# Performance work log

Hardware: AMD Instinct MI355X
Metric: run time of the kernel (lower is better)

## Reference

```python
import jax, jax.numpy as jnp
import numpy as np

B, DIM, H, W = 8, 128, 192, 192
HEADS = 4
WS = 8        # window size
SHIFT = 4     # shift size
N = WS * WS   # tokens per window
HD = DIM // HEADS
NW = (H // WS) * (W // WS)


def _relative_position_index(ws):
    coords = np.stack(np.meshgrid(np.arange(ws), np.arange(ws), indexing='ij'))  # (2,ws,ws)
    cf = coords.reshape(2, -1)                                                   # (2,N)
    rel = cf[:, :, None] - cf[:, None, :]                                        # (2,N,N)
    rel = rel.transpose(1, 2, 0).astype(np.int64)                                # (N,N,2)
    rel[:, :, 0] += ws - 1
    rel[:, :, 1] += ws - 1
    rel[:, :, 0] *= 2 * ws - 1
    return rel.sum(-1)  # (N,N)


def _window_partition_np(x, ws):
    b, h, w, c = x.shape
    x = x.reshape(b, h // ws, ws, w // ws, ws, c)
    return x.transpose(0, 1, 3, 2, 4, 5).reshape(-1, ws, ws, c)


def _shift_mask(h, w, ws, shift):
    img_mask = np.zeros((1, h, w, 1), dtype=np.float32)
    slices = (slice(0, -ws), slice(-ws, -shift), slice(-shift, None))
    cnt = 0
    for hs in slices:
        for wsl in slices:
            img_mask[:, hs, wsl, :] = cnt
            cnt += 1
    mw = _window_partition_np(img_mask, ws).reshape(-1, ws * ws)  # (nW, N)
    attn_mask = mw[:, None, :] - mw[:, :, None]                    # (nW, N, N)
    return np.where(attn_mask != 0, -100.0, 0.0).astype(np.float32)


_RPI = jnp.asarray(_relative_position_index(WS))   # (N,N) int
_MASK = jnp.asarray(_shift_mask(H, W, WS, SHIFT))  # (nW,N,N)


def setup_inputs() -> dict:
    key = jax.random.key(0)
    k0, k1, k2, k3 = jax.random.split(key, 4)
    return {
        'x': jax.random.normal(k0, (B, DIM, H, W), jnp.float32),
        'qkv_w': jax.random.normal(k1, (3 * DIM, DIM), jnp.float32) * 0.02,
        'qkv_b': jnp.zeros((3 * DIM,), jnp.float32),
        'proj_w': jax.random.normal(k2, (DIM, DIM), jnp.float32) * 0.02,
        'proj_b': jnp.zeros((DIM,), jnp.float32),
        'rpb_table': jax.random.normal(k3, ((2 * WS - 1) ** 2, HEADS), jnp.float32) * 0.02,
    }


def reference(x, qkv_w, qkv_b, proj_w, proj_b, rpb_table):
    scale = HD ** -0.5
    # (B,C,H,W) -> (B,H,W,C)
    xs = jnp.transpose(x, (0, 2, 3, 1))
    # cyclic shift
    xs = jnp.roll(xs, shift=(-SHIFT, -SHIFT), axis=(1, 2))
    # window partition -> (B*nW, N, C)
    win = xs.reshape(B, H // WS, WS, W // WS, WS, DIM)
    win = jnp.transpose(win, (0, 1, 3, 2, 4, 5)).reshape(B * NW, N, DIM)
    # qkv projection
    qkv = win @ qkv_w.T + qkv_b                                   # (B_,N,3C)
    qkv = qkv.reshape(B * NW, N, 3, HEADS, HD)
    qkv = jnp.transpose(qkv, (2, 0, 3, 1, 4))                     # (3,B_,h,N,d)
    q, k, v = qkv[0], qkv[1], qkv[2]
    attn = jnp.einsum('bhnd,bhmd->bhnm', q * scale, k)            # (B_,h,N,N)
    # relative position bias
    bias = rpb_table[_RPI.reshape(-1)].reshape(N, N, HEADS)
    bias = jnp.transpose(bias, (2, 0, 1))                         # (h,N,N)
    attn = attn + bias[None]
    # shift mask per window
    attn = attn.reshape(B, NW, HEADS, N, N) + _MASK[None, :, None]
    attn = jax.nn.softmax(attn.reshape(B * NW, HEADS, N, N), axis=-1)
    out = jnp.einsum('bhnm,bhmd->bhnd', attn, v)                  # (B_,h,N,d)
    out = jnp.transpose(out, (0, 2, 1, 3)).reshape(B * NW, N, DIM)
    out = out @ proj_w.T + proj_b
    # window reverse -> (B,H,W,C)
    out = out.reshape(B, H // WS, W // WS, WS, WS, DIM)
    out = jnp.transpose(out, (0, 1, 3, 2, 4, 5)).reshape(B, H, W, DIM)
    # reverse cyclic shift
    out = jnp.roll(out, shift=(SHIFT, SHIFT), axis=(1, 2))
    return jnp.transpose(out, (0, 3, 1, 2))  # (B,C,H,W)
```

## Files before the change

kernel.cpp:

```cpp
#include <hip/hip_runtime.h>

#define HIMG 192
#define HWSZ (192*192)
#define NWX  24

typedef __bf16 bf16;
typedef __bf16 bf16x4 __attribute__((ext_vector_type(4)));
typedef __bf16 bf16x8 __attribute__((ext_vector_type(8)));
typedef float  f32x4  __attribute__((ext_vector_type(4)));

#define MFMA(a,b,c) __builtin_amdgcn_mfma_f32_16x16x32_bf16((a),(b),(c),0,0,0)
#define SW(r) (((((r)&7) ^ ((((r)>>3)&1)<<2))) << 4)

static __device__ __forceinline__ bf16x8 ldg8(const float* p) {
    const float4 u = ((const float4*)p)[0];
    const float4 v = ((const float4*)p)[1];
    bf16x8 r;
    r[0]=(bf16)u.x; r[1]=(bf16)u.y; r[2]=(bf16)u.z; r[3]=(bf16)u.w;
    r[4]=(bf16)v.x; r[5]=(bf16)v.y; r[6]=(bf16)v.z; r[7]=(bf16)v.w;
    return r;
}
template<int WSB>
static __device__ __forceinline__ bf16x8 ldw(const float* wf, const bf16* wh, int off) {
    if (WSB) return *(const bf16x8*)(wh + off);
    return ldg8(wf + off);
}
static __device__ __forceinline__ bf16x4 pk4b(f32x4 v, float4 b) {
    bf16x4 r; r[0]=(bf16)(v[0]+b.x); r[1]=(bf16)(v[1]+b.y);
    r[2]=(bf16)(v[2]+b.z); r[3]=(bf16)(v[3]+b.w); return r;
}
static __device__ __forceinline__ bf16x4 pk4bs(f32x4 v, float4 b, float s) {
    bf16x4 r; r[0]=(bf16)((v[0]+b.x)*s); r[1]=(bf16)((v[1]+b.y)*s);
    r[2]=(bf16)((v[2]+b.z)*s); r[3]=(bf16)((v[3]+b.w)*s); return r;
}
static __device__ __forceinline__ bf16x4 pk4c(f32x4 v, float b) {
    bf16x4 r; r[0]=(bf16)(v[0]+b); r[1]=(bf16)(v[1]+b);
    r[2]=(bf16)(v[2]+b); r[3]=(bf16)(v[3]+b); return r;
}
static __device__ __forceinline__ bf16x4 pk4s(f32x4 v, float s) {
    bf16x4 r; r[0]=(bf16)(v[0]*s); r[1]=(bf16)(v[1]*s);
    r[2]=(bf16)(v[2]*s); r[3]=(bf16)(v[3]*s); return r;
}
static __device__ __forceinline__ bf16x4 pk4(f32x4 v) {
    bf16x4 r; r[0]=(bf16)v[0]; r[1]=(bf16)v[1]; r[2]=(bf16)v[2]; r[3]=(bf16)v[3]; return r;
}
static __device__ __forceinline__ bf16x8 cat8(bf16x4 a, bf16x4 b) {
    bf16x8 r; r[0]=a[0]; r[1]=a[1]; r[2]=a[2]; r[3]=a[3];
    r[4]=b[0]; r[5]=b[1]; r[6]=b[2]; r[7]=b[3]; return r;
}

__global__ __launch_bounds__(256) void setup_ws(const float* __restrict__ rpb,
                                                const float* __restrict__ qkv_w,
                                                const float* __restrict__ proj_w,
                                                float* __restrict__ wbias,
                                                bf16* __restrict__ hqkv,
                                                bf16* __restrict__ hproj,
                                                float* __restrict__ wbf,
                                                bf16* __restrict__ hqkvf,
                                                bf16* __restrict__ hprojf) {
    const int e = blockIdx.x * 256 + threadIdx.x;
    if (e < 16384) {
        const int h = e >> 12, i = (e >> 6) & 63, j = e & 63;
        const int dy = (i >> 3) - (j >> 3) + 7;
        const int dx = (i & 7)  - (j & 7)  + 7;
        wbias[e] = rpb[(dy * 15 + dx) * 4 + h];
    } else if (e < 65536) {
        const int i = e - 16384;
        hqkv[i] = (bf16)qkv_w[i];
    } else if (e < 81920) {
        const int i = e - 65536;
        hproj[i] = (bf16)proj_w[i];
    } else if (e < 98304) {
        const int t = e - 81920;
        const int r = t & 3, lane = (t >> 2) & 63;
        const int m = (t >> 8) & 3, n = (t >> 10) & 3, h = t >> 12;
        const int lo = lane & 15, hi = lane >> 4;
        const int i_ = n*16 + lo;
        const int j_ = (m >> 1)*32 + hi*8 + (m & 1)*4 + r;
        const int dy = (i_ >> 3) - (j_ >> 3) + 7;
        const int dx = (i_ & 7)  - (j_ & 7)  + 7;
        wbf[t] = rpb[(dy * 15 + dx) * 4 + h];
    } else if (e < 147456) {
        const int t = e - 98304;
        const int el = t & 7, lane = (t >> 3) & 63;
        const int a = (t >> 9) & 1, kb = (t >> 10) & 3;
        const int h = (t >> 12) & 3, ph = t >> 14;
        const int lo = lane & 15, hi = lane >> 4;
        const int prow = ((lo >> 2) << 3) + (lo & 3);
        const int row = (ph == 2) ? (256 + h*32 + a*16 + lo)
                                  : (ph*128 + h*32 + prow + a*4);
        const int col = kb*32 + hi*8 + el;
        hqkvf[t] = (bf16)qkv_w[row*128 + col];
    } else {
        const int t = e - 147456;
        const int el = t & 7, lane = (t >> 3) & 63;
        const int tA = (t >> 9) & 3, kb = (t >> 11) & 3, oh = t >> 13;
        const int lo = lane & 15, hi = lane >> 4;
        const int row = oh*64 + tA*16 + lo;
        const int col = kb*32 + hi*8 + el;
        hprojf[t] = (bf16)proj_w[row*128 + col];
    }
}

__global__ __launch_bounds__(256, 3)
void qkv_attn(const float* __restrict__ x, const float* __restrict__ qkv_b,
              const bf16* __restrict__ hqkvf, const float* __restrict__ wbf,
              bf16* __restrict__ obuf)
{
    __shared__ char sX[16384];
    const int tid  = threadIdx.x;
    const int lane = tid & 63;
    const int h    = tid >> 6;
    const int lo   = lane & 15;
    const int hi   = lane >> 4;

    const int bid   = blockIdx.x;
    const int batch = bid & 7;
    const int wrem  = bid >> 3;
    const int wy    = wrem / NWX;
    const int wx    = wrem - wy * NWX;
    const long xbase = (long)batch * 128 * HWSZ;

    const f32x4 FZ = {0.f, 0.f, 0.f, 0.f};
    const float SCALE = 0.17677669529663687f;
    const int prow = ((lo >> 2) << 3) + (lo & 3);

    {
        int hh = wy*8 + (lane >> 3) + 4; if (hh >= HIMG) hh -= HIMG;
        int ww = wx*8 + (lane & 7)  + 4; if (ww >= HIMG) ww -= HIMG;
        const float* xp = x + xbase + hh * HIMG + ww;
        char* const wp = sX + lane * 256;
        const int swz = SW(lane);
        #pragma unroll
        for (int g = 0; g < 4; ++g) {
            const int c0 = h*32 + g*8;
            bf16x8 v;
            #pragma unroll
            for (int e = 0; e < 8; ++e) v[e] = (bf16)xp[(c0 + e) * HWSZ];
            *(bf16x8*)(wp + ((2*c0) ^ swz)) = v;
        }
    }
    __syncthreads();

    const bf16* const wQ = hqkvf + h * 4096;
    const bf16* const wK = hqkvf + 16384 + h * 4096;
    const bf16* const wV = hqkvf + 32768 + h * 4096;

    bf16x8 qf[4], kf[4], vf[2][2];

    {
        f32x4 acc[2][4];
        #pragma unroll
        for (int a = 0; a < 2; ++a)
            #pragma unroll
            for (int n = 0; n < 4; ++n) acc[a][n] = FZ;
        #pragma unroll
        for (int kb = 0; kb < 4; ++kb) {
            bf16x8 xf[4];
            #pragma unroll
            for (int n = 0; n < 4; ++n) {
                const int row = n*16 + lo;
                xf[n] = *(const bf16x8*)(sX + row*256 + ((kb*64 + hi*16) ^ SW(row)));
            }
            const bf16x8 w0 = *(const bf16x8*)(wQ + (kb*2    )*512 + lane*8);
            const bf16x8 w1 = *(const bf16x8*)(wQ + (kb*2 + 1)*512 + lane*8);
            #pragma unroll
            for (int n = 0; n < 4; ++n) {
                acc[0][n] = MFMA(w0, xf[n], acc[0][n]);
                acc[1][n] = MFMA(w1, xf[n], acc[1][n]);
            }
        }
        const float4 b0 = *(const float4*)(qkv_b + h*32 + hi*8);
        const float4 b1 = *(const float4*)(qkv_b + h*32 + hi*8 + 4);
        #pragma unroll
        for (int n = 0; n < 4; ++n)
            qf[n] = cat8(pk4bs(acc[0][n], b0, SCALE), pk4bs(acc[1][n], b1, SCALE));
    }

    {
        f32x4 ak[2][4], av[4][2];
        #pragma unroll
        for (int m = 0; m < 4; ++m) {
            ak[0][m] = FZ; ak[1][m] = FZ; av[m][0] = FZ; av[m][1] = FZ;
        }
        #pragma unroll
        for (int kb = 0; kb < 4; ++kb) {
            bf16x8 xf[4];
            #pragma unroll
            for (int m = 0; m < 4; ++m) {
                const int row = (m >> 1)*32 + (m & 1)*4 + prow;
                xf[m] = *(const bf16x8*)(sX + row*256 + ((kb*64 + hi*16) ^ SW(row)));
            }
            const bf16x8 wk0 = *(const bf16x8*)(wK + (kb*2    )*512 + lane*8);
            const bf16x8 wk1 = *(const bf16x8*)(wK + (kb*2 + 1)*512 + lane*8);
            const bf16x8 wv0 = *(const bf16x8*)(wV + (kb*2    )*512 + lane*8);
            const bf16x8 wv1 = *(const bf16x8*)(wV + (kb*2 + 1)*512 + lane*8);
            #pragma unroll
            for (int m = 0; m < 4; ++m) {
                ak[0][m] = MFMA(wk0, xf[m], ak[0][m]);
                ak[1][m] = MFMA(wk1, xf[m], ak[1][m]);
                av[m][0] = MFMA(xf[m], wv0, av[m][0]);
                av[m][1] = MFMA(xf[m], wv1, av[m][1]);
            }
        }
        const float4 b0 = *(const float4*)(qkv_b + 128 + h*32 + hi*8);
        const float4 b1 = *(const float4*)(qkv_b + 128 + h*32 + hi*8 + 4);
        #pragma unroll
        for (int m = 0; m < 4; ++m)
            kf[m] = cat8(pk4b(ak[0][m], b0), pk4b(ak[1][m], b1));
        const float bv0 = qkv_b[256 + h*32 + lo];
        const float bv1 = qkv_b[256 + h*32 + 16 + lo];
        #pragma unroll
        for (int kb = 0; kb < 2; ++kb) {
            vf[0][kb] = cat8(pk4c(av[kb*2][0], bv0), pk4c(av[kb*2 + 1][0], bv0));
            vf[1][kb] = cat8(pk4c(av[kb*2][1], bv1), pk4c(av[kb*2 + 1][1], bv1));
        }
    }

    const bool ey = (wy == 23), ex = (wx == 23);
    const bool edge = ey || ex;
    const float* const wbh = wbf + h * 4096;
    bf16x8 pf[2][4];
    float rinv[4];
    #pragma unroll
    for (int n = 0; n < 4; ++n) {
        const int i_ = n*16 + lo;
        const int yi = i_ >> 3, xi = i_ & 7;
        const int ri = (ey ? (yi < 4 ? 1 : 2) : 0) * 3 + (ex ? (xi < 4 ? 1 : 2) : 0);
        f32x4 sc[4];
        #pragma unroll
        for (int m = 0; m < 4; ++m) {
            f32x4 ci = *(const f32x4*)(wbh + (n*4 + m)*256 + lane*4);
            if (edge) {
                #pragma unroll
                for (int r = 0; r < 4; ++r) {
                    const int j_ = (m >> 1)*32 + hi*8 + (m & 1)*4 + r;
                    const int yj = j_ >> 3, xj = j_ & 7;
                    const int rj = (ey ? (yj < 4 ? 1 : 2) : 0) * 3 + (ex ? (xj < 4 ? 1 : 2) : 0);
                    ci[r] += (ri != rj) ? -100.0f : 0.0f;
                }
            }
            sc[m] = MFMA(kf[m], qf[n], ci);
        }
        float mx = -1e30f;
        #pragma unroll
        for (int m = 0; m < 4; ++m)
            #pragma unroll
            for (int r = 0; r < 4; ++r) mx = fmaxf(mx, sc[m][r]);
        mx = fmaxf(mx, __shfl_xor(mx, 16));
        mx = fmaxf(mx, __shfl_xor(mx, 32));
        float sum = 0.f;
        #pragma unroll
        for (int m = 0; m < 4; ++m)
            #pragma unroll
            for (int r = 0; r < 4; ++r) {
                const float p = __expf(sc[m][r] - mx);
                sc[m][r] = p; sum += p;
            }
        sum += __shfl_xor(sum, 16);
        sum += __shfl_xor(sum, 32);
        rinv[n] = 1.0f / sum;
        pf[0][n] = cat8(pk4(sc[0]), pk4(sc[1]));
        pf[1][n] = cat8(pk4(sc[2]), pk4(sc[3]));
    }

    f32x4 o0[2][4];
    #pragma unroll
    for (int o = 0; o < 2; ++o)
        #pragma unroll
        for (int n = 0; n < 4; ++n) o0[o][n] = FZ;
    #pragma unroll
    for (int kb = 0; kb < 2; ++kb)
        #pragma unroll
        for (int o = 0; o < 2; ++o)
            #pragma unroll
            for (int n = 0; n < 4; ++n)
                o0[o][n] = MFMA(vf[o][kb], pf[kb][n], o0[o][n]);

    bf16* const ob = obuf + (size_t)bid * 8192 + h * 2048;
    #pragma unroll
    for (int n = 0; n < 4; ++n)
        #pragma unroll
        for (int o = 0; o < 2; ++o)
            *(bf16x4*)(ob + (n*2 + o)*256 + lane*4) = pk4s(o0[o][n], rinv[n]);
}

__global__ __launch_bounds__(512, 3)
void proj_rows(const bf16* __restrict__ obuf, const bf16* __restrict__ hprojf,
               const float* __restrict__ proj_b, float* __restrict__ out)
{
    __shared__ char sR[49152];
    const int tid  = threadIdx.x;
    const int lane = tid & 63;
    const int wv   = tid >> 6;
    const int lo   = lane & 15;
    const int hi   = lane >> 4;

    const int bid   = blockIdx.x;
    const int batch = bid & 7;
    const int hh    = bid >> 3;
    int hr = hh + 188; if (hr >= 192) hr -= 192;
    const int wy = hr >> 3, iy = hr & 7;
    const int n_ = iy >> 1;

    #pragma unroll
    for (int k = 0; k < 6; ++k) {
        const int i  = tid + k*512;
        const int wr = i >> 4;
        const int cc = i & 15;
        const int wxx = wr >> 3, ix = wr & 7;
        const int win = (wy*NWX + wxx)*8 + batch;
        const int lo2 = (iy & 1)*8 + ix;
        const int hg = cc >> 2, oo = (cc >> 1) & 1, hp = cc & 1;
        const bf16* bp = obuf + (size_t)win*8192 + hg*2048 + (n_*2 + oo)*256;
        const bf16x4 p0 = *(const bf16x4*)(bp + ((hp*2    )*16 + lo2)*4);
        const bf16x4 p1 = *(const bf16x4*)(bp + ((hp*2 + 1)*16 + lo2)*4);
        int wo = wr + 4; if (wo >= 192) wo -= 192;
        *(bf16x8*)(sR + wo*256 + ((cc*16) ^ SW(wo))) = cat8(p0, p1);
    }
    __syncthreads();

    const int q  = wv >> 1;
    const int oh = wv & 1;
    const f32x4 FZ = {0.f, 0.f, 0.f, 0.f};
    f32x4 acc[4][3];
    #pragma unroll
    for (int tA = 0; tA < 4; ++tA)
        #pragma unroll
        for (int tN = 0; tN < 3; ++tN) acc[tA][tN] = FZ;

    #pragma unroll
    for (int kb = 0; kb < 4; ++kb) {
        bf16x8 of[3];
        #pragma unroll
        for (int tN = 0; tN < 3; ++tN) {
            const int tok = q*48 + tN*16 + lo;
            of[tN] = *(const bf16x8*)(sR + tok*256 + ((kb*64 + hi*16) ^ SW(tok)));
        }
        bf16x8 wf[4];
        #pragma unroll
        for (int tA = 0; tA < 4; ++tA)
            wf[tA] = *(const bf16x8*)(hprojf + (size_t)(((oh*4 + kb)*4 + tA)*64 + lane)*8);
        #pragma unroll
        for (int tA = 0; tA < 4; ++tA)
            #pragma unroll
            for (int tN = 0; tN < 3; ++tN)
                acc[tA][tN] = MFMA(of[tN], wf[tA], acc[tA][tN]);
    }

    #pragma unroll
    for (int tA = 0; tA < 4; ++tA) {
        const int oc = oh*64 + tA*16 + lo;
        const float pb = proj_b[oc];
        float* const orow = out + (size_t)(batch*128 + oc) * HWSZ + hh*192;
        #pragma unroll
        for (int tN = 0; tN < 3; ++tN) {
            const int tb = q*48 + tN*16 + hi*4;
            float4 v;
            v.x = acc[tA][tN][0] + pb;
            v.y = acc[tA][tN][1] + pb;
            v.z = acc[tA][tN][2] + pb;
            v.w = acc[tA][tN][3] + pb;
            *(float4*)(orow + tb) = v;
        }
    }
}

template<int WSB>
__global__ __launch_bounds__(64, 2)
void swin_fused(const float* __restrict__ x, const float* __restrict__ qkv_w,
                const float* __restrict__ qkv_b, const float* __restrict__ proj_w,
                const float* __restrict__ proj_b, const float* __restrict__ rpb,
                const float* __restrict__ wb, const bf16* __restrict__ hqkv,
                const bf16* __restrict__ hproj, float* __restrict__ out)
{
    __shared__ char sX[16384];

    const int lane = threadIdx.x & 63;
    const int lo   = lane & 15;
    const int hi   = lane >> 4;

    const int bid   = blockIdx.x;
    const int batch = bid & 7;
    const int wrem  = bid >> 3;
    const int wy    = wrem / NWX;
    const int wx    = wrem - wy * NWX;
    const long xbase = (long)batch * 128 * HWSZ;

    const f32x4 FZ = {0.f, 0.f, 0.f, 0.f};
    const float SCALE = 0.17677669529663687f;
    const int prow = ((lo >> 2) << 3) + (lo & 3);

    {
        int hh = wy*8 + (lane >> 3) + 4; if (hh >= HIMG) hh -= HIMG;
        int ww = wx*8 + (lane & 7)  + 4; if (ww >= HIMG) ww -= HIMG;
        const float* xp = x + xbase + hh * HIMG + ww;
        char* const wp = sX + lane * 256;
        const int swz = SW(lane);
        #pragma unroll
        for (int g = 0; g < 16; ++g) {
            bf16x8 v;
            #pragma unroll
            for (int e = 0; e < 8; ++e) v[e] = (bf16)xp[(g*8 + e) * HWSZ];
            *(bf16x8*)(wp + ((16*g) ^ swz)) = v;
        }
    }

    const bool ey = (wy == 23), ex = (wx == 23);
    const bool edge = ey || ex;

    bf16x4 ob[4][2][4];

    #pragma unroll
    for (int h = 0; h < 4; ++h) {
        bf16x8 qf[4], kf[4];
        {
            f32x4 acc[2][4];
            #pragma unroll
            for (int a = 0; a < 2; ++a)
                #pragma unroll
                for (int n = 0; n < 4; ++n) acc[a][n] = FZ;
            #pragma unroll
            for (int kb = 0; kb < 4; ++kb) {
                bf16x8 xf[4];
                #pragma unroll
                for (int n = 0; n < 4; ++n) {
                    const int row = n*16 + lo;
                    xf[n] = *(const bf16x8*)(sX + row*256 + ((kb*64 + hi*16) ^ SW(row)));
                }
                const int coff = kb*32 + hi*8;
                const bf16x8 w0 = ldw<WSB>(qkv_w, hqkv, (h*32 + prow    ) * 128 + coff);
                const bf16x8 w1 = ldw<WSB>(qkv_w, hqkv, (h*32 + prow + 4) * 128 + coff);
                #pragma unroll
                for (int n = 0; n < 4; ++n) {
                    acc[0][n] = MFMA(w0, xf[n], acc[0][n]);
                    acc[1][n] = MFMA(w1, xf[n], acc[1][n]);
                }
            }
            const float4 b0 = *(const float4*)(qkv_b + h*32 + hi*8);
            const float4 b1 = *(const float4*)(qkv_b + h*32 + hi*8 + 4);
            #pragma unroll
            for (int n = 0; n < 4; ++n)
                qf[n] = cat8(pk4bs(acc[0][n], b0, SCALE), pk4bs(acc[1][n], b1, SCALE));
        }
        {
            f32x4 ak[2][4];
            #pragma unroll
            for (int a = 0; a < 2; ++a)
                #pragma unroll
                for (int m = 0; m < 4; ++m) ak[a][m] = FZ;
            #pragma unroll
            for (int kb = 0; kb < 4; ++kb) {
                bf16x8 xf[4];
                #pragma unroll
                for (int m = 0; m < 4; ++m) {
                    const int row = (m >> 1)*32 + (m & 1)*4 + prow;
                    xf[m] = *(const bf16x8*)(sX + row*256 + ((kb*64 + hi*16) ^ SW(row)));
                }
                const int coff = kb*32 + hi*8;
                const bf16x8 w0 = ldw<WSB>(qkv_w, hqkv, (128 + h*32 + prow    ) * 128 + coff);
                const bf16x8 w1 = ldw<WSB>(qkv_w, hqkv, (128 + h*32 + prow + 4) * 128 + coff);
                #pragma unroll
                for (int m = 0; m < 4; ++m) {
                    ak[0][m] = MFMA(w0, xf[m], ak[0][m]);
                    ak[1][m] = MFMA(w1, xf[m], ak[1][m]);
                }
            }
            const float4 b0 = *(const float4*)(qkv_b + 128 + h*32 + hi*8);
            const float4 b1 = *(const float4*)(qkv_b + 128 + h*32 + hi*8 + 4);
            #pragma unroll
            for (int m = 0; m < 4; ++m)
                kf[m] = cat8(pk4b(ak[0][m], b0), pk4b(ak[1][m], b1));
        }

        f32x4 s2[4][4];
        const float* wbh = wb + h * 4096;
        #pragma unroll
        for (int n = 0; n < 4; ++n) {
            const int i_ = n*16 + lo;
            const int yi = i_ >> 3, xi = i_ & 7;
            const int ri = (ey ? (yi < 4 ? 1 : 2) : 0) * 3 + (ex ? (xi < 4 ? 1 : 2) : 0);
            #pragma unroll
            for (int m = 0; m < 4; ++m) {
                const int j0 = (m >> 1)*32 + hi*8 + (m & 1)*4;
                f32x4 ci;
                if (WSB) ci = *(const f32x4*)(wbh + i_*64 + j0);
                else {
                    #pragma unroll
                    for (int r = 0; r < 4; ++r) {
                        const int j_ = j0 + r;
                        ci[r] = rpb[((yi - (j_ >> 3) + 7) * 15 + (xi - (j_ & 7) + 7)) * 4 + h];
                    }
                }
                if (edge) {
                    #pragma unroll
                    for (int r = 0; r < 4; ++r) {
                        const int j_ = j0 + r;
                        const int yj = j_ >> 3, xj = j_ & 7;
                        const int rj = (ey ? (yj < 4 ? 1 : 2) : 0) * 3 + (ex ? (xj < 4 ? 1 : 2) : 0);
                        ci[r] += (ri != rj) ? -100.0f : 0.0f;
                    }
                }
                s2[m][n] = MFMA(kf[m], qf[n], ci);
            }
        }
        float rinv[4];
        #pragma unroll
        for (int n = 0; n < 4; ++n) {
            float mx = -1e30f;
            #pragma unroll
            for (int m = 0; m < 4; ++m)
                #pragma unroll
                for (int r = 0; r < 4; ++r) mx = fmaxf(mx, s2[m][n][r]);
            mx = fmaxf(mx, __shfl_xor(mx, 16));
            mx = fmaxf(mx, __shfl_xor(mx, 32));
            float sum = 0.f;
            #pragma unroll
            for (int m = 0; m < 4; ++m)
                #pragma unroll
                for (int r = 0; r < 4; ++r) {
                    const float p = __expf(s2[m][n][r] - mx);
                    s2[m][n][r] = p; sum += p;
                }
            sum += __shfl_xor(sum, 16);
            sum += __shfl_xor(sum, 32);
            rinv[n] = 1.0f / sum;
        }
        bf16x8 pf[2][4];
        #pragma unroll
        for (int kb = 0; kb < 2; ++kb)
            #pragma unroll
            for (int n = 0; n < 4; ++n)
                pf[kb][n] = cat8(pk4(s2[kb*2][n]), pk4(s2[kb*2 + 1][n]));

        bf16x8 vf[2][2];
        {
            f32x4 av[4][2];
            #pragma unroll
            for (int m = 0; m < 4; ++m) { av[m][0] = FZ; av[m][1] = FZ; }
            #pragma unroll
            for (int kb = 0; kb < 4; ++kb) {
                bf16x8 xv[4];
                #pragma unroll
                for (int m = 0; m < 4; ++m) {
                    const int row = (m >> 1)*32 + (m & 1)*4 + prow;
                    xv[m] = *(const bf16x8*)(sX + row*256 + ((kb*64 + hi*16) ^ SW(row)));
                }
                const int coff = kb*32 + hi*8;
                const bf16x8 w0 = ldw<WSB>(qkv_w, hqkv, (256 + h*32 + lo)      * 128 + coff);
                const bf16x8 w1 = ldw<WSB>(qkv_w, hqkv, (256 + h*32 + 16 + lo) * 128 + coff);
                #pragma unroll
                for (int m = 0; m < 4; ++m) {
                    av[m][0] = MFMA(xv[m], w0, av[m][0]);
                    av[m][1] = MFMA(xv[m], w1, av[m][1]);
                }
            }
            const float bv0 = qkv_b[256 + h*32 + lo];
            const float bv1 = qkv_b[256 + h*32 + 16 + lo];
            #pragma unroll
            for (int kb = 0; kb < 2; ++kb) {
                vf[0][kb] = cat8(pk4c(av[kb*2][0], bv0), pk4c(av[kb*2 + 1][0], bv0));
                vf[1][kb] = cat8(pk4c(av[kb*2][1], bv1), pk4c(av[kb*2 + 1][1], bv1));
            }
        }
        {
            f32x4 o0[2][4];
            #pragma unroll
            for (int o = 0; o < 2; ++o)
                #pragma unroll
                for (int n = 0; n < 4; ++n) o0[o][n] = FZ;
            #pragma unroll
            for (int kb = 0; kb < 2; ++kb)
                #pragma unroll
                for (int o = 0; o < 2; ++o)
                    #pragma unroll
                    for (int n = 0; n < 4; ++n)
                        o0[o][n] = MFMA(vf[o][kb], pf[kb][n], o0[o][n]);
            #pragma unroll
            for (int o = 0; o < 2; ++o)
                #pragma unroll
                for (int n = 0; n < 4; ++n)
                    ob[h][o][n] = pk4s(o0[o][n], rinv[n]);
        }
    }

    #pragma unroll
    for (int h = 0; h < 4; ++h)
        #pragma unroll
        for (int o = 0; o < 2; ++o) {
            const int cb = h*64 + o*32 + hi*8;
            #pragma unroll
            for (int n = 0; n < 4; ++n) {
                const int t = n*16 + lo;
                *(bf16x4*)(sX + t*256 + (cb ^ SW(t))) = ob[h][o][n];
            }
        }

    #pragma unroll
    for (int c4 = 0; c4 < 4; ++c4) {
        f32x4 pr[2][4];
        #pragma unroll
        for (int a = 0; a < 2; ++a)
            #pragma unroll
            for (int n = 0; n < 4; ++n) pr[a][n] = FZ;
        #pragma unroll
        for (int kb = 0; kb < 4; ++kb) {
            bf16x8 af[4];
            #pragma unroll
            for (int n = 0; n < 4; ++n) {
                const int row = n*16 + lo;
                af[n] = *(const bf16x8*)(sX + row*256 + ((kb*64 + hi*16) ^ SW(row)));
            }
            const int coff = kb*32 + hi*8;
            const bf16x8 w0 = ldw<WSB>(proj_w, hproj, (c4*32 + lo)      * 128 + coff);
            const bf16x8 w1 = ldw<WSB>(proj_w, hproj, (c4*32 + 16 + lo) * 128 + coff);
            #pragma unroll
            for (int n = 0; n < 4; ++n) {
                pr[0][n] = MFMA(w0, af[n], pr[0][n]);
                pr[1][n] = MFMA(w1, af[n], pr[1][n]);
            }
        }
        #pragma unroll
        for (int a = 0; a < 2; ++a) {
            const int ocb = c4*32 + a*16 + hi*4;
            const float4 pb = *(const float4*)(proj_b + ocb);
            #pragma unroll
            for (int n = 0; n < 4; ++n) {
                const int t = n*16 + lo;
                int hh = wy*8 + (t >> 3) + 4; if (hh >= HIMG) hh -= HIMG;
                int ww = wx*8 + (t & 7)  + 4; if (ww >= HIMG) ww -= HIMG;
                float* op = out + (long)(batch*128 + ocb) * HWSZ + hh*HIMG + ww;
                op[0]      = pr[a][n][0] + pb.x;
                op[HWSZ]   = pr[a][n][1] + pb.y;
                op[2*HWSZ] = pr[a][n][2] + pb.z;
                op[3*HWSZ] = pr[a][n][3] + pb.w;
            }
        }
    }
}

extern "C" void kernel_launch(void* const* d_in, const int* in_sizes, int n_in,
                              void* d_out, int out_size, void* d_ws, size_t ws_size,
                              hipStream_t stream) {
    const float* x      = (const float*)d_in[0];
    const float* qkv_w  = (const float*)d_in[1];
    const float* qkv_b  = (const float*)d_in[2];
    const float* proj_w = (const float*)d_in[3];
    const float* proj_b = (const float*)d_in[4];
    const float* rpb    = (const float*)d_in[5];
    float* out = (float*)d_out;

    const size_t SETUP = 393216;
    const size_t OSZ   = (size_t)4608 * 16384;

    float* wbias = (float*)d_ws;
    bf16*  hqkv  = (bf16*)((char*)d_ws + 65536);
    bf16*  hproj = (bf16*)((char*)d_ws + 163840);
    float* wbf   = (float*)((char*)d_ws + 196608);
    bf16*  hqkvf = (bf16*)((char*)d_ws + 262144);
    bf16*  hprojf= (bf16*)((char*)d_ws + 360448);
    bf16*  obuf  = (bf16*)((char*)d_ws + SETUP);

    if (ws_size >= SETUP + OSZ) {
        setup_ws<<<640, 256, 0, stream>>>(rpb, qkv_w, proj_w, wbias, hqkv, hproj,
                                          wbf, hqkvf, hprojf);
        qkv_attn<<<4608, 256, 0, stream>>>(x, qkv_b, hqkvf, wbf, obuf);
        proj_rows<<<1536, 512, 0, stream>>>(obuf, hprojf, proj_b, out);
    } else if (ws_size >= SETUP) {
        setup_ws<<<640, 256, 0, stream>>>(rpb, qkv_w, proj_w, wbias, hqkv, hproj,
                                          wbf, hqkvf, hprojf);
        swin_fused<1><<<4608, 64, 0, stream>>>(x, qkv_w, qkv_b, proj_w, proj_b, rpb,
                                               wbias, hqkv, hproj, out);
    } else {
        swin_fused<0><<<4608, 64, 0, stream>>>(x, qkv_w, qkv_b, proj_w, proj_b, rpb,
                                               nullptr, nullptr, nullptr, out);
    }
}
```

Measured before the change: 157.9 us.

## Pre-transform input into bf16 windowed layout in a separate kernel

```diff
diff --git a/kernel.cpp b/kernel.cpp
--- a/kernel.cpp
+++ b/kernel.cpp
@@ -102,12 +102,57 @@
     }
 }
 
+__global__ __launch_bounds__(512, 3)
+void xform(const float* __restrict__ x, bf16* __restrict__ xw)
+{
+    __shared__ char sT[24576];
+    const int tid   = threadIdx.x;
+    const int bid   = blockIdx.x;
+    const int batch = bid & 7;
+    const int cq    = (bid >> 3) & 3;
+    const int wy    = bid >> 5;
+
+    #pragma unroll 1
+    for (int g = 0; g < 4; ++g) {
+        const int c0 = cq*32 + g*8;
+        #pragma unroll
+        for (int k = 0; k < 6; ++k) {
+            const int idx = tid + k*512;
+            const int ch  = idx / 384;
+            const int rem = idx - ch*384;
+            const int row = rem / 48;
+            const int c4  = rem - row*48;
+            int hr = wy*8 + row + 4; if (hr >= 192) hr -= 192;
+            const float4 v = *(const float4*)(x + (size_t)(batch*128 + c0 + ch)*HWSZ
+                                              + hr*HIMG + c4*4);
+            bf16x4 b4; b4[0]=(bf16)v.x; b4[1]=(bf16)v.y; b4[2]=(bf16)v.z; b4[3]=(bf16)v.w;
+            int cw0 = c4*4 - 4; if (cw0 < 0) cw0 += 192;
+            *(bf16x4*)(sT + ch*3072 + row*384 + cw0*2) = b4;
+        }
+        __syncthreads();
+        #pragma unroll
+        for (int j = 0; j < 3; ++j) {
+            const int otok = tid + j*512;
+            const int wx = otok >> 6;
+            const int t  = otok & 63;
+            const int iy = t >> 3, ix = t & 7;
+            const int cw = wx*8 + ix;
+            bf16x8 o;
+            #pragma unroll
+            for (int ch = 0; ch < 8; ++ch)
+                o[ch] = *(const bf16*)(sT + ch*3072 + iy*384 + cw*2);
+            const int win = (wy*NWX + wx)*8 + batch;
+            *(bf16x8*)(xw + (size_t)win*8192 + (cq*4 + g)*512 + t*8) = o;
+        }
+        __syncthreads();
+    }
+}
+
 __global__ __launch_bounds__(256, 3)
-void qkv_attn(const float* __restrict__ x, const float* __restrict__ qkv_b,
+void qkv_attn(const bf16* __restrict__ xw, const float* __restrict__ qkv_b,
               const bf16* __restrict__ hqkvf, const float* __restrict__ wbf,
               bf16* __restrict__ obuf)
 {
-    __shared__ char sX[16384];
     const int tid  = threadIdx.x;
     const int lane = tid & 63;
     const int h    = tid >> 6;
@@ -115,33 +160,15 @@
     const int hi   = lane >> 4;
 
     const int bid   = blockIdx.x;
-    const int batch = bid & 7;
     const int wrem  = bid >> 3;
     const int wy    = wrem / NWX;
     const int wx    = wrem - wy * NWX;
-    const long xbase = (long)batch * 128 * HWSZ;
 
     const f32x4 FZ = {0.f, 0.f, 0.f, 0.f};
     const float SCALE = 0.17677669529663687f;
     const int prow = ((lo >> 2) << 3) + (lo & 3);
 
-    {
-        int hh = wy*8 + (lane >> 3) + 4; if (hh >= HIMG) hh -= HIMG;
-        int ww = wx*8 + (lane & 7)  + 4; if (ww >= HIMG) ww -= HIMG;
-        const float* xp = x + xbase + hh * HIMG + ww;
-        char* const wp = sX + lane * 256;
-        const int swz = SW(lane);
-        #pragma unroll
-        for (int g = 0; g < 4; ++g) {
-            const int c0 = h*32 + g*8;
-            bf16x8 v;
-            #pragma unroll
-            for (int e = 0; e < 8; ++e) v[e] = (bf16)xp[(c0 + e) * HWSZ];
-            *(bf16x8*)(wp + ((2*c0) ^ swz)) = v;
-        }
-    }
-    __syncthreads();
-
+    const bf16* const xwb = xw + (size_t)bid * 8192;
     const bf16* const wQ = hqkvf + h * 4096;
     const bf16* const wK = hqkvf + 16384 + h * 4096;
     const bf16* const wV = hqkvf + 32768 + h * 4096;
@@ -158,10 +185,8 @@
         for (int kb = 0; kb < 4; ++kb) {
             bf16x8 xf[4];
             #pragma unroll
-            for (int n = 0; n < 4; ++n) {
-                const int row = n*16 + lo;
-                xf[n] = *(const bf16x8*)(sX + row*256 + ((kb*64 + hi*16) ^ SW(row)));
-            }
+            for (int n = 0; n < 4; ++n)
+                xf[n] = *(const bf16x8*)(xwb + (kb*4 + hi)*512 + (n*16 + lo)*8);
             const bf16x8 w0 = *(const bf16x8*)(wQ + (kb*2    )*512 + lane*8);
             const bf16x8 w1 = *(const bf16x8*)(wQ + (kb*2 + 1)*512 + lane*8);
             #pragma unroll
@@ -189,7 +214,7 @@
             #pragma unroll
             for (int m = 0; m < 4; ++m) {
                 const int row = (m >> 1)*32 + (m & 1)*4 + prow;
-                xf[m] = *(const bf16x8*)(sX + row*256 + ((kb*64 + hi*16) ^ SW(row)));
+                xf[m] = *(const bf16x8*)(xwb + (kb*4 + hi)*512 + row*8);
             }
             const bf16x8 wk0 = *(const bf16x8*)(wK + (kb*2    )*512 + lane*8);
             const bf16x8 wk1 = *(const bf16x8*)(wK + (kb*2 + 1)*512 + lane*8);
@@ -352,7 +377,7 @@
     for (int tA = 0; tA < 4; ++tA) {
         const int oc = oh*64 + tA*16 + lo;
         const float pb = proj_b[oc];
-        float* const orow = out + (size_t)(batch*128 + oc) * HWSZ + hh*192;
+        float* const orow = out + (size_t)(batch*128 + oc) * HWSZ + hh*HIMG;
         #pragma unroll
         for (int tN = 0; tN < 3; ++tN) {
             const int tb = q*48 + tN*16 + hi*4;
@@ -651,6 +676,7 @@
     float* out = (float*)d_out;
 
     const size_t SETUP = 393216;
+    const size_t XWSZ  = (size_t)4608 * 16384;
     const size_t OSZ   = (size_t)4608 * 16384;
 
     float* wbias = (float*)d_ws;
@@ -659,12 +685,14 @@
     float* wbf   = (float*)((char*)d_ws + 196608);
     bf16*  hqkvf = (bf16*)((char*)d_ws + 262144);
     bf16*  hprojf= (bf16*)((char*)d_ws + 360448);
-    bf16*  obuf  = (bf16*)((char*)d_ws + SETUP);
-
-    if (ws_size >= SETUP + OSZ) {
+    bf16*  xw    = (bf16*)((char*)d_ws + SETUP);
+    bf16*  obuf  = (bf16*)((char*)d_ws + SETUP + XWSZ);
+
+    if (ws_size >= SETUP + XWSZ + OSZ) {
         setup_ws<<<640, 256, 0, stream>>>(rpb, qkv_w, proj_w, wbias, hqkv, hproj,
                                           wbf, hqkvf, hprojf);
-        qkv_attn<<<4608, 256, 0, stream>>>(x, qkv_b, hqkvf, wbf, obuf);
+        xform<<<768, 512, 0, stream>>>(x, xw);
+        qkv_attn<<<4608, 256, 0, stream>>>(xw, qkv_b, hqkvf, wbf, obuf);
         proj_rows<<<1536, 512, 0, stream>>>(obuf, hprojf, proj_b, out);
     } else if (ws_size >= SETUP) {
         setup_ws<<<640, 256, 0, stream>>>(rpb, qkv_w, proj_w, wbias, hqkv, hproj,
```

Measured after the change: 192.1 us. 21.7% more time.
